# Kernel optimization log

Hardware: AMD Instinct MI355X
Metric: run time of the kernel (lower is better)

Reference implementation:

```python
import jax, jax.numpy as jnp
import numpy as np


def _conv3x3_replicate(x, w, b):
    # replicate (edge) padding then VALID 3x3 conv, NCHW / OIHW
    x = jnp.pad(x, ((0, 0), (0, 0), (1, 1), (1, 1)), mode='edge')
    y = jax.lax.conv_general_dilated(
        x, w, window_strides=(1, 1), padding='VALID',
        dimension_numbers=('NCHW', 'OIHW', 'NCHW'))
    return y + b[None, :, None, None]


def setup_inputs() -> dict:
    key = jax.random.key(0)
    ks = jax.random.split(key, 9)
    B, Cin, H, W = 8, 3, 256, 256
    Q, NC, Cout = 64, 32, 64
    x = jax.random.normal(ks[0], (B, Cin, H, W), dtype=jnp.float32)
    # Convx2: two 3x3 convs (replicate padding), then a 1x1 conv
    w1 = jax.random.normal(ks[1], (Q, Cin, 3, 3), dtype=jnp.float32) * (1.0 / np.sqrt(Cin * 9))
    b1 = jnp.zeros((Q,), jnp.float32)
    w2 = jax.random.normal(ks[2], (Q, Q, 3, 3), dtype=jnp.float32) * (1.0 / np.sqrt(Q * 9))
    b2 = jnp.zeros((Q,), jnp.float32)
    w3 = jax.random.normal(ks[3], (Q, Q, 1, 1), dtype=jnp.float32) * (1.0 / np.sqrt(Q))
    b3 = jnp.zeros((Q,), jnp.float32)
    cluster_mu = jax.random.normal(ks[4], (1, NC, Q, 1, 1), dtype=jnp.float32)
    cluster_label = jax.random.normal(ks[5], (Cout, NC), dtype=jnp.float32)
    return {'x': x, 'w1': w1, 'b1': b1, 'w2': w2, 'b2': b2, 'w3': w3, 'b3': b3,
            'cluster_mu': cluster_mu, 'cluster_label': cluster_label}


def reference(x, w1, b1, w2, b2, w3, b3, cluster_mu, cluster_label):
    # query encoder: Convx2 (conv3x3 -> ReLU -> conv3x3 -> ReLU) + 1x1 conv
    q = jax.nn.relu(_conv3x3_replicate(x, w1, b1))
    q = jax.nn.relu(_conv3x3_replicate(q, w2, b2))
    Qd = w3.shape[0]
    q = jnp.einsum('bchw,oc->bohw', q, w3.reshape(Qd, Qd)) + b3[None, :, None, None]  # (B,Q,H,W)
    # squared-distance logits, expanded form: -(||q||^2 - 2 q.mu + ||mu||^2)
    mu = cluster_mu.reshape(cluster_mu.shape[1], cluster_mu.shape[2])  # (NC,Q)
    qn = jnp.sum(q * q, axis=1)                       # (B,H,W)
    dot = jnp.einsum('bqhw,nq->bnhw', q, mu)          # (B,NC,H,W)
    mun = jnp.sum(mu * mu, axis=1)                    # (NC,)
    logit = -(qn[:, None] - 2.0 * dot + mun[None, :, None, None])
    attention = jax.nn.softmax(logit, axis=1)         # (B,NC,H,W)
    res = jnp.einsum('on,bnhw->bohw', cluster_label, attention)
    return res
```

## Files before the change

### kernel.cpp

```cpp
#include <hip/hip_runtime.h>

typedef _Float16 f16x8 __attribute__((ext_vector_type(8)));
typedef __fp16   half2 __attribute__((ext_vector_type(2)));
typedef float    f32x4 __attribute__((ext_vector_type(4)));

#define H_ 256
#define W_ 256

#define WS_W1S 0
#define WS_W2S 4096
#define WS_STG 77824

#define L_SQ1  0
#define L_W2S  39168
#define L_SX   63744
#define L_SQ2  0
#define LDS_SZ 76032

__global__ void repack_kernel(const float* __restrict__ w1, const float* __restrict__ b1,
                              const float* __restrict__ w2, const float* __restrict__ w3,
                              const float* __restrict__ b3, const float* __restrict__ mu,
                              const float* __restrict__ label, char* __restrict__ ws)
{
    int t = blockIdx.x * 256 + threadIdx.x;
    _Float16* w1s  = (_Float16*)(ws + WS_W1S);
    _Float16* w2s  = (_Float16*)(ws + WS_W2S);
    _Float16* mws  = (_Float16*)(ws + WS_STG);
    _Float16* labs = (_Float16*)(ws + WS_STG + 4096);
    float*    tn   = (float*)(ws + WS_STG + 8192);

    if (t < 2048) {
        int o = t >> 5, k = t & 31;
        float v = (k < 27) ? w1[o * 27 + k] : ((k == 27) ? b1[o] : 0.f);
        w1s[o * 32 + k] = (_Float16)v;
    }
    if (t < 36864) {
        int n = t / 576, rem = t % 576, c = rem / 9, tap = rem % 9;
        int chunk = c >> 5, k = c & 31;
        int slot = (k >> 3) ^ ((n ^ (n >> 2)) & 3);
        w2s[((chunk * 9 + tap) * 64 + n) * 32 + slot * 8 + (k & 7)] = (_Float16)w2[t];
    }
    if (t < 2048) {
        int n = t >> 6, c = t & 63;
        float s = 0.f;
        for (int o = 0; o < 64; ++o) s += mu[n * 64 + o] * w3[o * 64 + c];
        mws[n * 64 + c] = (_Float16)s;
    }
    if (t < 2048) {
        int o = t >> 5, cl = t & 31;
        labs[o * 32 + cl] = (_Float16)label[o * 32 + cl];
    }
    if (t < 32) {
        float d = 0.f, m2 = 0.f;
        for (int o = 0; o < 64; ++o) { float m = mu[t * 64 + o]; d += m * b3[o]; m2 += m * m; }
        tn[t] = 2.f * d - m2;
    }
}

__device__ __forceinline__ void stage_w2(const char* ws, char* smem, int chunk, int t0, int nt, int tid) {
    const uint4* s = (const uint4*)(ws + WS_W2S + (chunk * 9 + t0) * 4096);
    uint4* d = (uint4*)(smem + L_W2S + t0 * 4096);
    for (int i = tid; i < nt * 256; i += 512) d[i] = s[i];
}

template<int T0, int NT>
__device__ __forceinline__ void conv2_taps(const char* smem, f32x4 (&acc)[4][4],
                                           int wv, int ln, int lg, int swl) {
#pragma unroll
    for (int tt = 0; tt < NT; ++tt) {
        const int tap = T0 + tt;
        const int dy = tap / 3, dx = tap % 3;
        f16x8 wf[4], qf[4];
#pragma unroll
        for (int nb = 0; nb < 4; ++nb)
            wf[nb] = *(const f16x8*)(smem + L_W2S + ((tap * 64 + nb * 16 + ln) << 6) + ((lg ^ swl) << 4));
#pragma unroll
        for (int i = 0; i < 4; ++i) {
            int mb = wv * 4 + i;
            int pos = ((mb >> 1) + dy) * 34 + (mb & 1) * 16 + ln + dx;
            int sw = (pos ^ (pos >> 2)) & 3;
            qf[i] = *(const f16x8*)(smem + L_SQ1 + (pos << 6) + ((lg ^ sw) << 4));
        }
#pragma unroll
        for (int i = 0; i < 4; ++i)
#pragma unroll
            for (int nb = 0; nb < 4; ++nb)
                acc[i][nb] = __builtin_amdgcn_mfma_f32_16x16x32_f16(wf[nb], qf[i], acc[i][nb], 0, 0, 0);
    }
}

__global__ __launch_bounds__(512, 2) void fused_kernel(
    const float* __restrict__ x, const char* __restrict__ ws,
    const float* __restrict__ b2, float* __restrict__ out)
{
    __shared__ __align__(16) char smem[LDS_SZ];
    const int tid = threadIdx.x;
    const int lane = tid & 63;
    const int wv = tid >> 6;
    const int ln = lane & 15;
    const int lg = lane >> 4;
    const int swl = (ln ^ (ln >> 2)) & 3;
    const int w0 = blockIdx.x * 32, h0 = blockIdx.y * 16, bz = blockIdx.z;

    {
        float* sx = (float*)(smem + L_SX);
        for (int i = tid; i < 2160; i += 512) {
            int ci = i / 720, rem = i - ci * 720;
            int r = rem / 36, c = rem - (rem / 36) * 36;
            int gy = min(max(h0 - 2 + r, 0), H_ - 1);
            int gx = min(max(w0 - 2 + c, 0), W_ - 1);
            sx[i] = x[((bz * 3 + ci) * H_ + gy) * W_ + gx];
        }
    }
    float b2v[4][4];
#pragma unroll
    for (int nb = 0; nb < 4; ++nb)
#pragma unroll
        for (int jr = 0; jr < 4; ++jr)
            b2v[nb][jr] = b2[nb * 16 + lg * 4 + jr];

    int koff[8]; float kcv[8]; int kvalid[8];
#pragma unroll
    for (int j = 0; j < 8; ++j) {
        int k = lg * 8 + j;
        int ci = (k * 57) >> 9;
        int r  = k - 9 * ci;
        int dy = (r * 22) >> 6;
        int dx = r - 3 * dy;
        koff[j]   = ci * 720 + dy * 36 + dx;
        kvalid[j] = (k < 27);
        kcv[j]    = (k == 27) ? 1.0f : 0.0f;
    }

    __syncthreads();

    const f16x8* w1sp = (const f16x8*)(ws + WS_W1S);
    const float* sxp = (const float*)(smem + L_SX);

    f32x4 acc[4][4];
#pragma unroll
    for (int i = 0; i < 4; ++i)
#pragma unroll
        for (int nb = 0; nb < 4; ++nb)
            acc[i][nb] = (f32x4){b2v[nb][0], b2v[nb][1], b2v[nb][2], b2v[nb][3]};

    f16x8 bfr[5];
    int wrow[5], wswp[5], wok[5];

    stage_w2(ws, smem, 0, 0, 6, tid);
    {
        f16x8 w1f[2];
#pragma unroll
        for (int nb2 = 0; nb2 < 2; ++nb2)
            w1f[nb2] = w1sp[(nb2 * 16 + ln) * 4 + lg];
#pragma unroll
        for (int t = 0; t < 5; ++t) {
            int pb = wv + 8 * t;
            if (pb >= 39) break;
            int pos_w = pb * 16 + ln;
            int pos = min(pos_w, 611);
            int sy = (pos * 241) >> 13;
            int sp = pos - sy * 34;
            int by = min(max(h0 - 1 + sy, 0), H_ - 1) - (h0 - 1);
            int bx = min(max(w0 - 1 + sp, 0), W_ - 1) - (w0 - 1);
            int base = by * 36 + bx;
            float g[8];
#pragma unroll
            for (int j = 0; j < 8; ++j) {
                float v = sxp[base + koff[j]];
                g[j] = kvalid[j] ? v : kcv[j];
            }
            union { half2 h2[4]; f16x8 f; } u;
#pragma unroll
            for (int jj = 0; jj < 4; ++jj)
                u.h2[jj] = __builtin_amdgcn_cvt_pkrtz(g[2 * jj], g[2 * jj + 1]);
            bfr[t] = u.f;
            wrow[t] = pos_w * 64 + ((lg & 1) << 3);
            wswp[t] = (pos_w ^ (pos_w >> 2)) & 3;
            wok[t]  = (pos_w < 612);
#pragma unroll
            for (int nb2 = 0; nb2 < 2; ++nb2) {
                f32x4 c0 = {0.f, 0.f, 0.f, 0.f};
                c0 = __builtin_amdgcn_mfma_f32_16x16x32_f16(w1f[nb2], bfr[t], c0, 0, 0, 0);
                union { half2 h2[2]; uint2 u2; } pk;
                pk.h2[0] = __builtin_amdgcn_cvt_pkrtz(fmaxf(c0[0], 0.f), fmaxf(c0[1], 0.f));
                pk.h2[1] = __builtin_amdgcn_cvt_pkrtz(fmaxf(c0[2], 0.f), fmaxf(c0[3], 0.f));
                int s2 = 2 * nb2 + (lg >> 1);
                if (wok[t])
                    *(uint2*)(smem + L_SQ1 + wrow[t] + ((s2 ^ wswp[t]) << 4)) = pk.u2;
            }
        }
    }
    __syncthreads();

    stage_w2(ws, smem, 0, 6, 3, tid);
    conv2_taps<0, 6>(smem, acc, wv, ln, lg, swl);
    __syncthreads();

    stage_w2(ws, smem, 1, 0, 6, tid);
    conv2_taps<6, 3>(smem, acc, wv, ln, lg, swl);
    __syncthreads();

    stage_w2(ws, smem, 1, 6, 3, tid);
    {
        f16x8 w1f[2];
#pragma unroll
        for (int nb2 = 0; nb2 < 2; ++nb2)
            w1f[nb2] = w1sp[(32 + nb2 * 16 + ln) * 4 + lg];
#pragma unroll
        for (int t = 0; t < 5; ++t) {
            int pb = wv + 8 * t;
            if (pb >= 39) break;
#pragma unroll
            for (int nb2 = 0; nb2 < 2; ++nb2) {
                f32x4 c0 = {0.f, 0.f, 0.f, 0.f};
                c0 = __builtin_amdgcn_mfma_f32_16x16x32_f16(w1f[nb2], bfr[t], c0, 0, 0, 0);
                union { half2 h2[2]; uint2 u2; } pk;
                pk.h2[0] = __builtin_amdgcn_cvt_pkrtz(fmaxf(c0[0], 0.f), fmaxf(c0[1], 0.f));
                pk.h2[1] = __builtin_amdgcn_cvt_pkrtz(fmaxf(c0[2], 0.f), fmaxf(c0[3], 0.f));
                int s2 = 2 * nb2 + (lg >> 1);
                if (wok[t])
                    *(uint2*)(smem + L_SQ1 + wrow[t] + ((s2 ^ wswp[t]) << 4)) = pk.u2;
            }
        }
    }
    __syncthreads();

    conv2_taps<0, 9>(smem, acc, wv, ln, lg, swl);
    __syncthreads();

    float tnr[8];
#pragma unroll
    for (int nb2 = 0; nb2 < 2; ++nb2)
#pragma unroll
        for (int jr = 0; jr < 4; ++jr)
            tnr[nb2 * 4 + jr] = *(const float*)(ws + WS_STG + 8192 + ((nb2 * 16 + lg * 4 + jr) << 2));

#pragma unroll
    for (int i = 0; i < 4; ++i) {
        int pix = (wv * 4 + i) * 16 + ln;
        int sw = pix & 7;
#pragma unroll
        for (int nb = 0; nb < 4; ++nb) {
            union { half2 h2[2]; uint2 u2; } pk;
            pk.h2[0] = __builtin_amdgcn_cvt_pkrtz(fmaxf(acc[i][nb][0], 0.f), fmaxf(acc[i][nb][1], 0.f));
            pk.h2[1] = __builtin_amdgcn_cvt_pkrtz(fmaxf(acc[i][nb][2], 0.f), fmaxf(acc[i][nb][3], 0.f));
            int s2 = 2 * nb + (lg >> 1);
            *(uint2*)(smem + L_SQ2 + (pix << 7) + ((s2 ^ sw) << 4) + ((lg & 1) << 3)) = pk.u2;
        }
    }

    f32x4 acc3[4][2];
#pragma unroll
    for (int i = 0; i < 4; ++i)
#pragma unroll
        for (int nb2 = 0; nb2 < 2; ++nb2) acc3[i][nb2] = (f32x4){0.f, 0.f, 0.f, 0.f};
#pragma unroll
    for (int ks = 0; ks < 2; ++ks) {
        f16x8 mwf[2], af[4];
#pragma unroll
        for (int nb2 = 0; nb2 < 2; ++nb2)
            mwf[nb2] = *(const f16x8*)(ws + WS_STG + ((nb2 * 16 + ln) << 7) + ((ks * 4 + lg) << 4));
#pragma unroll
        for (int i = 0; i < 4; ++i) {
            int pix = (wv * 4 + i) * 16 + ln;
            af[i] = *(const f16x8*)(smem + L_SQ2 + (pix << 7) + (((ks * 4 + lg) ^ (pix & 7)) << 4));
        }
#pragma unroll
        for (int i = 0; i < 4; ++i)
#pragma unroll
            for (int nb2 = 0; nb2 < 2; ++nb2)
                acc3[i][nb2] = __builtin_amdgcn_mfma_f32_16x16x32_f16(mwf[nb2], af[i], acc3[i][nb2], 0, 0, 0);
    }

#pragma unroll
    for (int i = 0; i < 4; ++i) {
        float l[8];
#pragma unroll
        for (int nb2 = 0; nb2 < 2; ++nb2)
#pragma unroll
            for (int jr = 0; jr < 4; ++jr)
                l[nb2 * 4 + jr] = 2.f * acc3[i][nb2][jr] + tnr[nb2 * 4 + jr];
        float mx = l[0];
#pragma unroll
        for (int j = 1; j < 8; ++j) mx = fmaxf(mx, l[j]);
        mx = fmaxf(mx, __shfl_xor(mx, 16));
        mx = fmaxf(mx, __shfl_xor(mx, 32));
        float ssum = 0.f;
#pragma unroll
        for (int j = 0; j < 8; ++j) { l[j] = __expf(l[j] - mx); ssum += l[j]; }
        ssum += __shfl_xor(ssum, 16);
        ssum += __shfl_xor(ssum, 32);
        float inv = 1.f / ssum;
        int lr = i * 16 + ln;
        int pix = wv * 64 + lr;
        int sw = (pix ^ (pix >> 2)) & 3;
#pragma unroll
        for (int nb2 = 0; nb2 < 2; ++nb2) {
            union { half2 h2[2]; uint2 u2; } pk;
            pk.h2[0] = __builtin_amdgcn_cvt_pkrtz(l[nb2 * 4 + 0] * inv, l[nb2 * 4 + 1] * inv);
            pk.h2[1] = __builtin_amdgcn_cvt_pkrtz(l[nb2 * 4 + 2] * inv, l[nb2 * 4 + 3] * inv);
            int s2 = 2 * nb2 + (lg >> 1);
            *(uint2*)(smem + L_SQ2 + (wv << 13) + (lr << 6) + ((s2 ^ sw) << 4) + ((lg & 1) << 3)) = pk.u2;
        }
    }

    f16x8 lf[4], pf[4];
#pragma unroll
    for (int nb = 0; nb < 4; ++nb)
        lf[nb] = *(const f16x8*)(ws + WS_STG + 4096 + ((nb * 16 + ln) << 6) + (lg << 4));
#pragma unroll
    for (int i = 0; i < 4; ++i) {
        int lr = i * 16 + ln;
        int pix = wv * 64 + lr;
        int sw = (pix ^ (pix >> 2)) & 3;
        pf[i] = *(const f16x8*)(smem + L_SQ2 + (wv << 13) + (lr << 6) + ((lg ^ sw) << 4));
    }
#pragma unroll
    for (int i = 0; i < 4; ++i) {
        int mb = wv * 4 + i;
        int base = (bz * 64 * H_ + (h0 + (mb >> 1))) * W_ + w0 + (mb & 1) * 16 + ln;
#pragma unroll
        for (int nb = 0; nb < 4; ++nb) {
            f32x4 c4 = {0.f, 0.f, 0.f, 0.f};
            c4 = __builtin_amdgcn_mfma_f32_16x16x32_f16(lf[nb], pf[i], c4, 0, 0, 0);
#pragma unroll
            for (int jr = 0; jr < 4; ++jr)
                out[base + (nb * 16 + lg * 4 + jr) * (H_ * W_)] = c4[jr];
        }
    }
}

extern "C" void kernel_launch(void* const* d_in, const int* in_sizes, int n_in,
                              void* d_out, int out_size, void* d_ws, size_t ws_size,
                              hipStream_t stream) {
    const float* x  = (const float*)d_in[0];
    const float* w1 = (const float*)d_in[1];
    const float* b1 = (const float*)d_in[2];
    const float* w2 = (const float*)d_in[3];
    const float* b2 = (const float*)d_in[4];
    const float* w3 = (const float*)d_in[5];
    const float* b3 = (const float*)d_in[6];
    const float* mu = (const float*)d_in[7];
    const float* lb = (const float*)d_in[8];
    float* out = (float*)d_out;
    char* ws = (char*)d_ws;

    repack_kernel<<<144, 256, 0, stream>>>(w1, b1, w2, w3, b3, mu, lb, ws);
    dim3 grid(W_ / 32, H_ / 16, 8);
    fused_kernel<<<grid, 512, 0, stream>>>(x, ws, b2, out);
}
```

Baseline: 86.84 us.

## Shrink fused conv tile to 16x8 with 256 threads and full-chunk weight staging

Shrinks the per-block output tile from 32x16 to 16x8 pixels, runs 256 threads per block and quadruples the grid. LDS use drops, so more blocks can be resident per CU. Each channel half of the w2 weights is now staged in one step instead of two partial stages, which removes intermediate barriers. The input halo is stored as fp16 in shared memory. The cost is a larger relative halo overhead: more recomputation of conv1 at tile borders and more redundant loads of weights per output pixel.

```diff
diff --git a/kernel.cpp b/kernel.cpp
--- a/kernel.cpp
+++ b/kernel.cpp
@@ -12,10 +12,10 @@
 #define WS_STG 77824
 
 #define L_SQ1  0
-#define L_W2S  39168
-#define L_SX   63744
+#define L_W2S  11520
+#define L_SXH  48384
 #define L_SQ2  0
-#define LDS_SZ 76032
+#define LDS_SZ 49824
 
 __global__ void repack_kernel(const float* __restrict__ w1, const float* __restrict__ b1,
                               const float* __restrict__ w2, const float* __restrict__ w3,
@@ -57,39 +57,38 @@
     }
 }
 
-__device__ __forceinline__ void stage_w2(const char* ws, char* smem, int chunk, int t0, int nt, int tid) {
-    const uint4* s = (const uint4*)(ws + WS_W2S + (chunk * 9 + t0) * 4096);
-    uint4* d = (uint4*)(smem + L_W2S + t0 * 4096);
-    for (int i = tid; i < nt * 256; i += 512) d[i] = s[i];
+__device__ __forceinline__ void stage_w2(const char* ws, char* smem, int chunk_off, int tid) {
+    const uint4* s = (const uint4*)(ws + WS_W2S + chunk_off);
+    uint4* d = (uint4*)(smem + L_W2S);
+    for (int i = tid; i < 2304; i += 256) d[i] = s[i];
 }
 
 template<int T0, int NT>
-__device__ __forceinline__ void conv2_taps(const char* smem, f32x4 (&acc)[4][4],
+__device__ __forceinline__ void conv2_taps(const char* smem, f32x4 (&acc)[2][4],
                                            int wv, int ln, int lg, int swl) {
 #pragma unroll
     for (int tt = 0; tt < NT; ++tt) {
         const int tap = T0 + tt;
         const int dy = tap / 3, dx = tap % 3;
-        f16x8 wf[4], qf[4];
+        f16x8 wf[4], qf[2];
 #pragma unroll
         for (int nb = 0; nb < 4; ++nb)
             wf[nb] = *(const f16x8*)(smem + L_W2S + ((tap * 64 + nb * 16 + ln) << 6) + ((lg ^ swl) << 4));
 #pragma unroll
-        for (int i = 0; i < 4; ++i) {
-            int mb = wv * 4 + i;
-            int pos = ((mb >> 1) + dy) * 34 + (mb & 1) * 16 + ln + dx;
+        for (int i = 0; i < 2; ++i) {
+            int pos = (wv * 2 + i + dy) * 18 + ln + dx;
             int sw = (pos ^ (pos >> 2)) & 3;
             qf[i] = *(const f16x8*)(smem + L_SQ1 + (pos << 6) + ((lg ^ sw) << 4));
         }
 #pragma unroll
-        for (int i = 0; i < 4; ++i)
+        for (int i = 0; i < 2; ++i)
 #pragma unroll
             for (int nb = 0; nb < 4; ++nb)
                 acc[i][nb] = __builtin_amdgcn_mfma_f32_16x16x32_f16(wf[nb], qf[i], acc[i][nb], 0, 0, 0);
     }
 }
 
-__global__ __launch_bounds__(512, 2) void fused_kernel(
+__global__ __launch_bounds__(256, 2) void fused_kernel(
     const float* __restrict__ x, const char* __restrict__ ws,
     const float* __restrict__ b2, float* __restrict__ out)
 {
@@ -100,84 +99,72 @@
     const int ln = lane & 15;
     const int lg = lane >> 4;
     const int swl = (ln ^ (ln >> 2)) & 3;
-    const int w0 = blockIdx.x * 32, h0 = blockIdx.y * 16, bz = blockIdx.z;
-
+    const int w0 = blockIdx.x * 16, h0 = blockIdx.y * 8, bz = blockIdx.z;
+
+    stage_w2(ws, smem, 0, tid);
     {
-        float* sx = (float*)(smem + L_SX);
-        for (int i = tid; i < 2160; i += 512) {
-            int ci = i / 720, rem = i - ci * 720;
-            int r = rem / 36, c = rem - (rem / 36) * 36;
+        _Float16* sxh = (_Float16*)(smem + L_SXH);
+        for (int i = tid; i < 720; i += 256) {
+            int ci = i / 240, rem = i - ci * 240;
+            int r = rem / 20, c = rem - (rem / 20) * 20;
             int gy = min(max(h0 - 2 + r, 0), H_ - 1);
             int gx = min(max(w0 - 2 + c, 0), W_ - 1);
-            sx[i] = x[((bz * 3 + ci) * H_ + gy) * W_ + gx];
-        }
-    }
-    float b2v[4][4];
-#pragma unroll
-    for (int nb = 0; nb < 4; ++nb)
-#pragma unroll
-        for (int jr = 0; jr < 4; ++jr)
-            b2v[nb][jr] = b2[nb * 16 + lg * 4 + jr];
-
-    int koff[8]; float kcv[8]; int kvalid[8];
-#pragma unroll
-    for (int j = 0; j < 8; ++j) {
-        int k = lg * 8 + j;
-        int ci = (k * 57) >> 9;
-        int r  = k - 9 * ci;
-        int dy = (r * 22) >> 6;
-        int dx = r - 3 * dy;
-        koff[j]   = ci * 720 + dy * 36 + dx;
-        kvalid[j] = (k < 27);
-        kcv[j]    = (k == 27) ? 1.0f : 0.0f;
-    }
-
+            sxh[i] = (_Float16)x[((bz * 3 + ci) * H_ + gy) * W_ + gx];
+        }
+    }
     __syncthreads();
 
     const f16x8* w1sp = (const f16x8*)(ws + WS_W1S);
-    const float* sxp = (const float*)(smem + L_SX);
-
-    f32x4 acc[4][4];
-#pragma unroll
-    for (int i = 0; i < 4; ++i)
-#pragma unroll
-        for (int nb = 0; nb < 4; ++nb)
-            acc[i][nb] = (f32x4){b2v[nb][0], b2v[nb][1], b2v[nb][2], b2v[nb][3]};
-
-    f16x8 bfr[5];
-    int wrow[5], wswp[5], wok[5];
-
-    stage_w2(ws, smem, 0, 0, 6, tid);
+    const unsigned short* sxu = (const unsigned short*)(smem + L_SXH);
+
+    f32x4 acc[2][4];
+#pragma unroll
+    for (int nb = 0; nb < 4; ++nb) {
+        float4 bv = *(const float4*)(b2 + nb * 16 + lg * 4);
+#pragma unroll
+        for (int i = 0; i < 2; ++i) acc[i][nb] = (f32x4){bv.x, bv.y, bv.z, bv.w};
+    }
+
+    f16x8 bfr[3];
+    int wrow[3];
+
     {
+        int koff[8]; unsigned short kcst[8]; int kvalid[8];
+#pragma unroll
+        for (int j = 0; j < 8; ++j) {
+            int k = lg * 8 + j;
+            int ci = (k * 57) >> 9;
+            int r  = k - 9 * ci;
+            int dy = (r * 22) >> 6;
+            int dx = r - 3 * dy;
+            koff[j]   = ci * 240 + dy * 20 + dx;
+            kvalid[j] = (k < 27);
+            kcst[j]   = (k == 27) ? 0x3C00 : 0;
+        }
         f16x8 w1f[2];
 #pragma unroll
         for (int nb2 = 0; nb2 < 2; ++nb2)
             w1f[nb2] = w1sp[(nb2 * 16 + ln) * 4 + lg];
 #pragma unroll
-        for (int t = 0; t < 5; ++t) {
-            int pb = wv + 8 * t;
-            if (pb >= 39) break;
+        for (int t = 0; t < 3; ++t) {
+            int pb = wv + 4 * t;
             int pos_w = pb * 16 + ln;
-            int pos = min(pos_w, 611);
-            int sy = (pos * 241) >> 13;
-            int sp = pos - sy * 34;
+            int pos = min(pos_w, 179);
+            int sy = (pos * 3641) >> 16;
+            int sp = pos - sy * 18;
             int by = min(max(h0 - 1 + sy, 0), H_ - 1) - (h0 - 1);
             int bx = min(max(w0 - 1 + sp, 0), W_ - 1) - (w0 - 1);
-            int base = by * 36 + bx;
-            float g[8];
+            int base = by * 20 + bx;
+            union { unsigned short us[8]; f16x8 f; } u;
 #pragma unroll
             for (int j = 0; j < 8; ++j) {
-                float v = sxp[base + koff[j]];
-                g[j] = kvalid[j] ? v : kcv[j];
+                unsigned short v = sxu[kvalid[j] ? base + koff[j] : 0];
+                u.us[j] = kvalid[j] ? v : kcst[j];
             }
-            union { half2 h2[4]; f16x8 f; } u;
-#pragma unroll
-            for (int jj = 0; jj < 4; ++jj)
-                u.h2[jj] = __builtin_amdgcn_cvt_pkrtz(g[2 * jj], g[2 * jj + 1]);
             bfr[t] = u.f;
             wrow[t] = pos_w * 64 + ((lg & 1) << 3);
-            wswp[t] = (pos_w ^ (pos_w >> 2)) & 3;
-            wok[t]  = (pos_w < 612);
+            int wswp = (pos_w ^ (pos_w >> 2)) & 3;
+            int wok = (pos_w < 180);
 #pragma unroll
             for (int nb2 = 0; nb2 < 2; ++nb2) {
                 f32x4 c0 = {0.f, 0.f, 0.f, 0.f};
@@ -186,31 +173,27 @@
                 pk.h2[0] = __builtin_amdgcn_cvt_pkrtz(fmaxf(c0[0], 0.f), fmaxf(c0[1], 0.f));
                 pk.h2[1] = __builtin_amdgcn_cvt_pkrtz(fmaxf(c0[2], 0.f), fmaxf(c0[3], 0.f));
                 int s2 = 2 * nb2 + (lg >> 1);
-                if (wok[t])
-                    *(uint2*)(smem + L_SQ1 + wrow[t] + ((s2 ^ wswp[t]) << 4)) = pk.u2;
+                if (wok)
+                    *(uint2*)(smem + L_SQ1 + wrow[t] + ((s2 ^ wswp) << 4)) = pk.u2;
             }
         }
     }
     __syncthreads();
 
-    stage_w2(ws, smem, 0, 6, 3, tid);
-    conv2_taps<0, 6>(smem, acc, wv, ln, lg, swl);
-    __syncthreads();
-
-    stage_w2(ws, smem, 1, 0, 6, tid);
-    conv2_taps<6, 3>(smem, acc, wv, ln, lg, swl);
-    __syncthreads();
-
-    stage_w2(ws, smem, 1, 6, 3, tid);
+    conv2_taps<0, 9>(smem, acc, wv, ln, lg, swl);
+    __syncthreads();
+
+    stage_w2(ws, smem, 36864, tid);
     {
         f16x8 w1f[2];
 #pragma unroll
         for (int nb2 = 0; nb2 < 2; ++nb2)
             w1f[nb2] = w1sp[(32 + nb2 * 16 + ln) * 4 + lg];
 #pragma unroll
-        for (int t = 0; t < 5; ++t) {
-            int pb = wv + 8 * t;
-            if (pb >= 39) break;
+        for (int t = 0; t < 3; ++t) {
+            int pos_w = wrow[t] >> 6;
+            int wswp = (pos_w ^ (pos_w >> 2)) & 3;
+            int wok = (pos_w < 180);
 #pragma unroll
             for (int nb2 = 0; nb2 < 2; ++nb2) {
                 f32x4 c0 = {0.f, 0.f, 0.f, 0.f};
@@ -219,8 +202,8 @@
                 pk.h2[0] = __builtin_amdgcn_cvt_pkrtz(fmaxf(c0[0], 0.f), fmaxf(c0[1], 0.f));
                 pk.h2[1] = __builtin_amdgcn_cvt_pkrtz(fmaxf(c0[2], 0.f), fmaxf(c0[3], 0.f));
                 int s2 = 2 * nb2 + (lg >> 1);
-                if (wok[t])
-                    *(uint2*)(smem + L_SQ1 + wrow[t] + ((s2 ^ wswp[t]) << 4)) = pk.u2;
+                if (wok)
+                    *(uint2*)(smem + L_SQ1 + wrow[t] + ((s2 ^ wswp) << 4)) = pk.u2;
             }
         }
     }
@@ -237,8 +220,8 @@
             tnr[nb2 * 4 + jr] = *(const float*)(ws + WS_STG + 8192 + ((nb2 * 16 + lg * 4 + jr) << 2));
 
 #pragma unroll
-    for (int i = 0; i < 4; ++i) {
-        int pix = (wv * 4 + i) * 16 + ln;
+    for (int i = 0; i < 2; ++i) {
+        int pix = (wv * 2 + i) * 16 + ln;
         int sw = pix & 7;
 #pragma unroll
         for (int nb = 0; nb < 4; ++nb) {
@@ -250,31 +233,31 @@
         }
     }
 
-    f32x4 acc3[4][2];
-#pragma unroll
-    for (int i = 0; i < 4; ++i)
+    f32x4 acc3[2][2];
+#pragma unroll
+    for (int i = 0; i < 2; ++i)
 #pragma unroll
         for (int nb2 = 0; nb2 < 2; ++nb2) acc3[i][nb2] = (f32x4){0.f, 0.f, 0.f, 0.f};
 #pragma unroll
     for (int ks = 0; ks < 2; ++ks) {
-        f16x8 mwf[2], af[4];
+        f16x8 mwf[2], af[2];
 #pragma unroll
         for (int nb2 = 0; nb2 < 2; ++nb2)
             mwf[nb2] = *(const f16x8*)(ws + WS_STG + ((nb2 * 16 + ln) << 7) + ((ks * 4 + lg) << 4));
 #pragma unroll
-        for (int i = 0; i < 4; ++i) {
-            int pix = (wv * 4 + i) * 16 + ln;
+        for (int i = 0; i < 2; ++i) {
+            int pix = (wv * 2 + i) * 16 + ln;
             af[i] = *(const f16x8*)(smem + L_SQ2 + (pix << 7) + (((ks * 4 + lg) ^ (pix & 7)) << 4));
         }
 #pragma unroll
-        for (int i = 0; i < 4; ++i)
+        for (int i = 0; i < 2; ++i)
 #pragma unroll
             for (int nb2 = 0; nb2 < 2; ++nb2)
                 acc3[i][nb2] = __builtin_amdgcn_mfma_f32_16x16x32_f16(mwf[nb2], af[i], acc3[i][nb2], 0, 0, 0);
     }
 
 #pragma unroll
-    for (int i = 0; i < 4; ++i) {
+    for (int i = 0; i < 2; ++i) {
         float l[8];
 #pragma unroll
         for (int nb2 = 0; nb2 < 2; ++nb2)
@@ -293,33 +276,32 @@
         ssum += __shfl_xor(ssum, 32);
         float inv = 1.f / ssum;
         int lr = i * 16 + ln;
-        int pix = wv * 64 + lr;
-        int sw = (pix ^ (pix >> 2)) & 3;
+        int prow = wv * 64 + lr;
+        int sw = (prow ^ (prow >> 2)) & 3;
 #pragma unroll
         for (int nb2 = 0; nb2 < 2; ++nb2) {
             union { half2 h2[2]; uint2 u2; } pk;
             pk.h2[0] = __builtin_amdgcn_cvt_pkrtz(l[nb2 * 4 + 0] * inv, l[nb2 * 4 + 1] * inv);
             pk.h2[1] = __builtin_amdgcn_cvt_pkrtz(l[nb2 * 4 + 2] * inv, l[nb2 * 4 + 3] * inv);
             int s2 = 2 * nb2 + (lg >> 1);
-            *(uint2*)(smem + L_SQ2 + (wv << 13) + (lr << 6) + ((s2 ^ sw) << 4) + ((lg & 1) << 3)) = pk.u2;
-        }
-    }
-
-    f16x8 lf[4], pf[4];
+            *(uint2*)(smem + L_SQ2 + (wv << 12) + (lr << 6) + ((s2 ^ sw) << 4) + ((lg & 1) << 3)) = pk.u2;
+        }
+    }
+
+    f16x8 lf[4], pf[2];
 #pragma unroll
     for (int nb = 0; nb < 4; ++nb)
         lf[nb] = *(const f16x8*)(ws + WS_STG + 4096 + ((nb * 16 + ln) << 6) + (lg << 4));
 #pragma unroll
-    for (int i = 0; i < 4; ++i) {
+    for (int i = 0; i < 2; ++i) {
         int lr = i * 16 + ln;
-        int pix = wv * 64 + lr;
-        int sw = (pix ^ (pix >> 2)) & 3;
-        pf[i] = *(const f16x8*)(smem + L_SQ2 + (wv << 13) + (lr << 6) + ((lg ^ sw) << 4));
-    }
-#pragma unroll
-    for (int i = 0; i < 4; ++i) {
-        int mb = wv * 4 + i;
-        int base = (bz * 64 * H_ + (h0 + (mb >> 1))) * W_ + w0 + (mb & 1) * 16 + ln;
+        int prow = wv * 64 + lr;
+        int sw = (prow ^ (prow >> 2)) & 3;
+        pf[i] = *(const f16x8*)(smem + L_SQ2 + (wv << 12) + (lr << 6) + ((lg ^ sw) << 4));
+    }
+#pragma unroll
+    for (int i = 0; i < 2; ++i) {
+        int base = (bz * 64 * H_ + (h0 + wv * 2 + i)) * W_ + w0 + ln;
 #pragma unroll
         for (int nb = 0; nb < 4; ++nb) {
             f32x4 c4 = {0.f, 0.f, 0.f, 0.f};
@@ -347,6 +329,6 @@
     char* ws = (char*)d_ws;
 
     repack_kernel<<<144, 256, 0, stream>>>(w1, b1, w2, w3, b3, mu, lb, ws);
-    dim3 grid(W_ / 32, H_ / 16, 8);
-    fused_kernel<<<grid, 512, 0, stream>>>(x, ws, b2, out);
-}
+    dim3 grid(W_ / 16, H_ / 8, 8);
+    fused_kernel<<<grid, 256, 0, stream>>>(x, ws, b2, out);
+}
```

After: 87.79 us. Within noise of the previous version (+1.1%).
